# Kernel optimization log

Hardware: AMD Instinct MI355X
Metric: run time of the kernel (lower is better)

## Reference

```python
import jax, jax.numpy as jnp
import numpy as np

NEG = -1000000000.0


def setup_inputs() -> dict:
    key = jax.random.key(0)
    k1, k2, k3, k4, k5 = jax.random.split(key, 5)
    B, T, D, Q = 8, 2048, 1024, 128
    x = jax.random.normal(k1, (B, T, D), dtype=jnp.float32)
    attn_mask = jax.random.randint(k2, (B, T), 0, 2).astype(jnp.bool_)
    s = 1.0 / np.sqrt(D)
    Wq = jax.random.normal(k3, (Q, D), dtype=jnp.float32) * s
    Wk = jax.random.normal(k4, (Q, D), dtype=jnp.float32) * s
    Wv = jax.random.normal(k5, (Q, D), dtype=jnp.float32) * s
    return {"x": x, "attn_mask": attn_mask, "Wq": Wq, "Wk": Wk, "Wv": Wv}


def reference(x, attn_mask, Wq, Wk, Wv):
    # x: (B,T,D); W*: (Q,D) torch Linear weights (y = x @ W.T)
    q = jnp.einsum('btd,qd->btq', x, Wq)
    k = jnp.einsum('btd,qd->btq', x, Wk)
    v = jnp.einsum('btd,qd->btq', x, Wv)
    logits = jnp.einsum('btq,bsq->bts', q, k)  # (B,T,T), no 1/sqrt(d) scaling (matches source)
    m = attn_mask[:, None, :]  # (B,1,T) broadcasts over query dim, == repeat(1,T,1)
    logits = jnp.where(m, logits, NEG)
    A = jax.nn.softmax(logits, axis=-1)
    A = jnp.where(m, A, 0.0)
    return jnp.einsum('bts,bsq->btq', A, v)
```

## Files before the change

### kernel.cpp

```cpp
#include <hip/hip_runtime.h>
#include <hip/hip_bf16.h>
#include <hip/hip_fp16.h>

typedef _Float16 half8 __attribute__((ext_vector_type(8)));
typedef _Float16 half4v __attribute__((ext_vector_type(4)));
typedef float float4v __attribute__((ext_vector_type(4)));

#define MFMA_F16(a, b, c) __builtin_amdgcn_mfma_f32_16x16x32_f16((a), (b), (c), 0, 0, 0)

#define GLDS16(gp, lp) \
    __builtin_amdgcn_global_load_lds((const __attribute__((address_space(1))) unsigned int*)(gp), \
                                     (__attribute__((address_space(3))) unsigned int*)(lp), 16, 0, 0)

#define BATCH 8
#define SEQ   2048
#define DIM   1024
#define QD    128
#define BT    (BATCH * SEQ)
#define NSPLIT 4
#define KSPAN (SEQ / NSPLIT)

__device__ __forceinline__ float dpp_max16(float x) {
    int v;
    v = __builtin_amdgcn_update_dpp(0, __float_as_int(x), 0xB1, 0xF, 0xF, false);
    x = fmaxf(x, __int_as_float(v));
    v = __builtin_amdgcn_update_dpp(0, __float_as_int(x), 0x4E, 0xF, 0xF, false);
    x = fmaxf(x, __int_as_float(v));
    v = __builtin_amdgcn_update_dpp(0, __float_as_int(x), 0x141, 0xF, 0xF, false);
    x = fmaxf(x, __int_as_float(v));
    v = __builtin_amdgcn_update_dpp(0, __float_as_int(x), 0x140, 0xF, 0xF, false);
    x = fmaxf(x, __int_as_float(v));
    return x;
}

__global__ __launch_bounds__(256) void cvt_x_kernel(const float* __restrict__ s,
                                                    _Float16* __restrict__ d) {
    int i = blockIdx.x * 256 + threadIdx.x;
    float4 f = ((const float4*)s)[i];
    half4v h = {(_Float16)f.x, (_Float16)f.y, (_Float16)f.z, (_Float16)f.w};
    ((half4v*)d)[i] = h;
}

__global__ __launch_bounds__(256) void cvt_w_kernel(const float* __restrict__ Wq,
                                                    const float* __restrict__ Wk,
                                                    const float* __restrict__ Wv,
                                                    _Float16* __restrict__ Wh) {
    const float* src = (blockIdx.y == 0) ? Wq : ((blockIdx.y == 1) ? Wk : Wv);
    int i = blockIdx.x * 256 + threadIdx.x;
    float4 f = ((const float4*)src)[i];
    half4v h = {(_Float16)f.x, (_Float16)f.y, (_Float16)f.z, (_Float16)f.w};
    ((half4v*)(Wh + (size_t)blockIdx.y * QD * DIM))[i] = h;
}

__global__ __launch_bounds__(256, 3) void proj_kernel(
    const _Float16* __restrict__ xh,
    const _Float16* __restrict__ Wh,
    _Float16* __restrict__ q_out,
    _Float16* __restrict__ k_out,
    _Float16* __restrict__ vt_out)
{
    __shared__ _Float16 As[64 * 64];
    __shared__ _Float16 Bs[128 * 64];

    const int tid  = threadIdx.x;
    const int lane = tid & 63;
    const int wave = tid >> 6;
    const int quad = lane >> 4;
    const int l15  = lane & 15;
    const int wr   = wave >> 1;
    const int wc   = wave & 1;

    const int which = blockIdx.y;
    const _Float16* W = Wh + (size_t)which * QD * DIM;
    const int row0 = blockIdx.x * 64;

    float4v acc[2][4];
#pragma unroll
    for (int rf = 0; rf < 2; rf++)
#pragma unroll
        for (int n = 0; n < 4; n++)
            acc[rf][n] = (float4v){0.f, 0.f, 0.f, 0.f};

    for (int kk = 0; kk < DIM; kk += 64) {
        __syncthreads();
#pragma unroll
        for (int c = 0; c < 2; c++) {
            int ci = wave * 128 + c * 64 + lane;
            int r  = ci >> 3;
            int g  = (ci & 7) ^ (r & 7);
            GLDS16(xh + (size_t)(row0 + r) * DIM + kk + g * 8, &As[(wave * 128 + c * 64) * 8]);
        }
#pragma unroll
        for (int c = 0; c < 4; c++) {
            int ci = wave * 256 + c * 64 + lane;
            int r  = ci >> 3;
            int g  = (ci & 7) ^ (r & 7);
            GLDS16(W + (size_t)r * DIM + kk + g * 8, &Bs[(wave * 256 + c * 64) * 8]);
        }
        __syncthreads();

        half8 af[2][2], bf[4][2];
#pragma unroll
        for (int rf = 0; rf < 2; rf++)
#pragma unroll
            for (int kc = 0; kc < 2; kc++) {
                int r = wr * 32 + rf * 16 + l15;
                int g = (kc * 4 + quad) ^ (r & 7);
                af[rf][kc] = *(const half8*)&As[r * 64 + g * 8];
            }
#pragma unroll
        for (int n = 0; n < 4; n++)
#pragma unroll
            for (int kc = 0; kc < 2; kc++) {
                int r = wc * 64 + n * 16 + l15;
                int g = (kc * 4 + quad) ^ (r & 7);
                bf[n][kc] = *(const half8*)&Bs[r * 64 + g * 8];
            }
#pragma unroll
        for (int kc = 0; kc < 2; kc++)
#pragma unroll
            for (int rf = 0; rf < 2; rf++)
#pragma unroll
                for (int n = 0; n < 4; n++)
                    acc[rf][n] = MFMA_F16(af[rf][kc], bf[n][kc], acc[rf][n]);
    }

    if (which == 2) {
#pragma unroll
        for (int rf = 0; rf < 2; rf++) {
            int grow0 = row0 + wr * 32 + rf * 16 + quad * 4;
            int b  = grow0 >> 11;
            int t0 = grow0 & 2047;
#pragma unroll
            for (int n = 0; n < 4; n++) {
                int col = wc * 64 + n * 16 + l15;
                half4v h;
#pragma unroll
                for (int r = 0; r < 4; r++) h[r] = (_Float16)acc[rf][n][r];
                *(half4v*)&vt_out[((size_t)(b * QD + col)) * SEQ + t0] = h;
            }
        }
    } else {
        _Float16* out = (which == 0) ? q_out : k_out;
#pragma unroll
        for (int rf = 0; rf < 2; rf++) {
            int grow0 = row0 + wr * 32 + rf * 16 + quad * 4;
#pragma unroll
            for (int n = 0; n < 4; n++) {
                int col = wc * 64 + n * 16 + l15;
#pragma unroll
                for (int r = 0; r < 4; r++)
                    out[(size_t)(grow0 + r) * QD + col] = (_Float16)acc[rf][n][r];
            }
        }
    }
}

__global__ __launch_bounds__(256, 2) void attn_kernel(
    const _Float16* __restrict__ q,
    const _Float16* __restrict__ k,
    const _Float16* __restrict__ vt,
    const int* __restrict__ mask,
    _Float16* __restrict__ Op,
    float2* __restrict__ ml)
{
    __shared__ _Float16 Ks[64 * 128];
    __shared__ _Float16 Vs[128 * 64];
    __shared__ _Float16 Ps[4 * 32 * 64];
    __shared__ int Ms[64];

    const int tid  = threadIdx.x;
    const int lane = tid & 63;
    const int wave = tid >> 6;
    const int quad = lane >> 4;
    const int l15  = lane & 15;

    const int b  = blockIdx.y;
    const int z  = blockIdx.z;
    const int rowbase = blockIdx.x * 128 + wave * 32;

    half8 qf[2][4];
#pragma unroll
    for (int rf = 0; rf < 2; rf++) {
        const _Float16* qrow = q + ((size_t)(b * SEQ + rowbase + rf * 16 + l15)) * QD + quad * 8;
#pragma unroll
        for (int kc = 0; kc < 4; kc++)
            qf[rf][kc] = *(const half8*)(qrow + kc * 32);
    }

    const half8 onesv = {(_Float16)1, (_Float16)1, (_Float16)1, (_Float16)1,
                         (_Float16)1, (_Float16)1, (_Float16)1, (_Float16)1};

    float4v oacc[2][8];
#pragma unroll
    for (int rf = 0; rf < 2; rf++)
#pragma unroll
        for (int n = 0; n < 8; n++)
            oacc[rf][n] = (float4v){0.f, 0.f, 0.f, 0.f};
    float4v lacc[2] = {(float4v){0.f, 0.f, 0.f, 0.f}, (float4v){0.f, 0.f, 0.f, 0.f}};
    float mrow[2][4];
#pragma unroll
    for (int rf = 0; rf < 2; rf++)
#pragma unroll
        for (int r = 0; r < 4; r++) mrow[rf][r] = -1e30f;

    _Float16* Pw = &Ps[wave * 32 * 64];

    for (int sb = z * KSPAN; sb < z * KSPAN + KSPAN; sb += 64) {
        __syncthreads();
#pragma unroll
        for (int c = 0; c < 4; c++) {
            int ci = wave * 256 + c * 64 + lane;
            int r  = ci >> 4;
            int gs = ci & 15;
            int g  = (gs & 8) | ((gs ^ r) & 7);
            GLDS16(k + ((size_t)(b * SEQ + sb + r)) * QD + g * 8, &Ks[(wave * 256 + c * 64) * 8]);
        }
#pragma unroll
        for (int c = 0; c < 4; c++) {
            int ci = wave * 256 + c * 64 + lane;
            int r  = ci >> 3;
            int g  = ((ci & 7) ^ r) & 7;
            GLDS16(vt + ((size_t)(b * QD + r)) * SEQ + sb + g * 8, &Vs[(wave * 256 + c * 64) * 8]);
        }
        if (tid < 64) Ms[tid] = mask[b * SEQ + sb + tid];
        __syncthreads();

        float4v sacc[2][4];
#pragma unroll
        for (int rf = 0; rf < 2; rf++)
#pragma unroll
            for (int j = 0; j < 4; j++)
                sacc[rf][j] = (float4v){0.f, 0.f, 0.f, 0.f};
#pragma unroll
        for (int kc = 0; kc < 4; kc++) {
            half8 kf[4];
#pragma unroll
            for (int j = 0; j < 4; j++) {
                int r  = j * 16 + l15;
                int g  = kc * 4 + quad;
                int gs = (g & 8) | ((g ^ r) & 7);
                kf[j] = *(const half8*)&Ks[r * 128 + gs * 8];
            }
#pragma unroll
            for (int rf = 0; rf < 2; rf++)
#pragma unroll
                for (int j = 0; j < 4; j++)
                    sacc[rf][j] = MFMA_F16(qf[rf][kc], kf[j], sacc[rf][j]);
        }

        float alpha[2][4];
#pragma unroll
        for (int rf = 0; rf < 2; rf++) {
            float rmax[4] = {-1e30f, -1e30f, -1e30f, -1e30f};
#pragma unroll
            for (int j = 0; j < 4; j++) {
                bool m_ok = (Ms[j * 16 + l15] != 0);
#pragma unroll
                for (int r = 0; r < 4; r++) {
                    float s = m_ok ? sacc[rf][j][r] : -1e30f;
                    sacc[rf][j][r] = s;
                    rmax[r] = fmaxf(rmax[r], s);
                }
            }
#pragma unroll
            for (int r = 0; r < 4; r++) {
                float rm = dpp_max16(rmax[r]);
                float mnew = fmaxf(mrow[rf][r], rm);
                alpha[rf][r] = __expf(mrow[rf][r] - mnew);
                mrow[rf][r] = mnew;
            }
        }

#pragma unroll
        for (int rf = 0; rf < 2; rf++)
#pragma unroll
            for (int j = 0; j < 4; j++) {
                int col = j * 16 + l15;
                int gc  = col >> 3;
#pragma unroll
                for (int r = 0; r < 4; r++) {
                    int m  = rf * 16 + quad * 4 + r;
                    int gs = (gc ^ m) & 7;
                    float s = sacc[rf][j][r];
                    float p = (s > -1e29f) ? __expf(s - mrow[rf][r]) : 0.f;
                    Pw[m * 64 + gs * 8 + (col & 7)] = (_Float16)p;
                }
            }

#pragma unroll
        for (int rf = 0; rf < 2; rf++) {
#pragma unroll
            for (int n = 0; n < 8; n++)
#pragma unroll
                for (int r = 0; r < 4; r++)
                    oacc[rf][n][r] *= alpha[rf][r];
#pragma unroll
            for (int r = 0; r < 4; r++) lacc[rf][r] *= alpha[rf][r];
        }

#pragma unroll
        for (int kc = 0; kc < 2; kc++) {
            half8 pf[2];
#pragma unroll
            for (int rf = 0; rf < 2; rf++) {
                int m  = rf * 16 + l15;
                int gs = ((kc * 4 + quad) ^ m) & 7;
                pf[rf] = *(const half8*)&Pw[m * 64 + gs * 8];
            }
#pragma unroll
            for (int n = 0; n < 8; n++) {
                int r  = n * 16 + l15;
                int gs = ((kc * 4 + quad) ^ r) & 7;
                half8 vf = *(const half8*)&Vs[r * 64 + gs * 8];
#pragma unroll
                for (int rf = 0; rf < 2; rf++)
                    oacc[rf][n] = MFMA_F16(pf[rf], vf, oacc[rf][n]);
            }
#pragma unroll
            for (int rf = 0; rf < 2; rf++)
                lacc[rf] = MFMA_F16(pf[rf], onesv, lacc[rf]);
        }
    }

    _Float16* Oz = Op + (size_t)z * BT * QD;
#pragma unroll
    for (int rf = 0; rf < 2; rf++) {
#pragma unroll
        for (int n = 0; n < 8; n++) {
            int col = n * 16 + l15;
#pragma unroll
            for (int r = 0; r < 4; r++) {
                int row = rowbase + rf * 16 + quad * 4 + r;
                Oz[((size_t)(b * SEQ + row)) * QD + col] = (_Float16)oacc[rf][n][r];
            }
        }
        if (l15 == 0) {
#pragma unroll
            for (int r = 0; r < 4; r++) {
                int row = rowbase + rf * 16 + quad * 4 + r;
                ml[(size_t)z * BT + b * SEQ + row] = make_float2(mrow[rf][r], lacc[rf][r]);
            }
        }
    }
}

__global__ __launch_bounds__(256) void merge_kernel(
    const _Float16* __restrict__ Op,
    const float2* __restrict__ ml,
    float* __restrict__ out)
{
    int gid = blockIdx.x * 256 + threadIdx.x;
    int row = gid >> 4;
    int c8  = (gid & 15) * 8;

    float2 a[NSPLIT];
    float m = -3.0e38f;
#pragma unroll
    for (int s = 0; s < NSPLIT; s++) { a[s] = ml[(size_t)s * BT + row]; m = fmaxf(m, a[s].x); }
    float sc[NSPLIT];
    float denom = 0.f;
#pragma unroll
    for (int s = 0; s < NSPLIT; s++) { sc[s] = __expf(a[s].x - m); denom += sc[s] * a[s].y; }
    float inv = (denom > 0.f) ? (1.0f / denom) : 0.f;

    float acc[8] = {0, 0, 0, 0, 0, 0, 0, 0};
#pragma unroll
    for (int s = 0; s < NSPLIT; s++) {
        half8 o = *(const half8*)&Op[(size_t)s * BT * QD + (size_t)row * QD + c8];
#pragma unroll
        for (int e = 0; e < 8; e++) acc[e] += (float)o[e] * sc[s];
    }
    float4 lo = make_float4(acc[0] * inv, acc[1] * inv, acc[2] * inv, acc[3] * inv);
    float4 hi = make_float4(acc[4] * inv, acc[5] * inv, acc[6] * inv, acc[7] * inv);
    *(float4*)&out[(size_t)row * QD + c8] = lo;
    *(float4*)&out[(size_t)row * QD + c8 + 4] = hi;
}

extern "C" void kernel_launch(void* const* d_in, const int* in_sizes, int n_in,
                              void* d_out, int out_size, void* d_ws, size_t ws_size,
                              hipStream_t stream) {
    const float* x    = (const float*)d_in[0];
    const int*   mask = (const int*)d_in[1];
    const float* Wq   = (const float*)d_in[2];
    const float* Wk   = (const float*)d_in[3];
    const float* Wv   = (const float*)d_in[4];
    float* out = (float*)d_out;

    char* p = (char*)d_ws;
    _Float16* xh  = (_Float16*)p; p += (size_t)BT * DIM * 2;
    _Float16* Wh  = (_Float16*)p; p += (size_t)3 * QD * DIM * 2;
    _Float16* qb  = (_Float16*)p; p += (size_t)BT * QD * 2;
    _Float16* kb  = (_Float16*)p; p += (size_t)BT * QD * 2;
    _Float16* vtb = (_Float16*)p; p += (size_t)BT * QD * 2;
    _Float16* Op  = (_Float16*)p; p += (size_t)NSPLIT * BT * QD * 2;
    float2*   ml  = (float2*)p;

    cvt_x_kernel<<<dim3(BT * DIM / 4 / 256), 256, 0, stream>>>(x, xh);
    cvt_w_kernel<<<dim3(QD * DIM / 4 / 256, 3), 256, 0, stream>>>(Wq, Wk, Wv, Wh);
    proj_kernel<<<dim3(BT / 64, 3), 256, 0, stream>>>(xh, Wh, qb, kb, vtb);
    attn_kernel<<<dim3(SEQ / 128, BATCH, NSPLIT), 256, 0, stream>>>(qb, kb, vtb, mask, Op, ml);
    merge_kernel<<<dim3(BT * 16 / 256), 256, 0, stream>>>(Op, ml, out);
}
```

Before: 164.9 us.

## Fuse x fp32-to-fp16 conversion into projection and use additive mask bias

Removes the standalone x conversion kernel and its fp16 workspace buffer. The projection kernel now loads fp32 x rows into registers, converts them, and writes them to swizzled LDS, replacing the async global-to-LDS copies for the A tile. This drops a full read/write pass over x and one launch. The cost is that each of the three projection blocks reads fp32 x itself, and those register loads replace async LDS loads. Separately, the attention mask is stored as an additive 0/-1e30 bias, which removes the selects before the max and the exp.

```diff
diff --git a/kernel.cpp b/kernel.cpp
--- a/kernel.cpp
+++ b/kernel.cpp
@@ -33,14 +33,6 @@
     return x;
 }
 
-__global__ __launch_bounds__(256) void cvt_x_kernel(const float* __restrict__ s,
-                                                    _Float16* __restrict__ d) {
-    int i = blockIdx.x * 256 + threadIdx.x;
-    float4 f = ((const float4*)s)[i];
-    half4v h = {(_Float16)f.x, (_Float16)f.y, (_Float16)f.z, (_Float16)f.w};
-    ((half4v*)d)[i] = h;
-}
-
 __global__ __launch_bounds__(256) void cvt_w_kernel(const float* __restrict__ Wq,
                                                     const float* __restrict__ Wk,
                                                     const float* __restrict__ Wv,
@@ -53,7 +45,7 @@
 }
 
 __global__ __launch_bounds__(256, 3) void proj_kernel(
-    const _Float16* __restrict__ xh,
+    const float* __restrict__ x,
     const _Float16* __restrict__ Wh,
     _Float16* __restrict__ q_out,
     _Float16* __restrict__ k_out,
@@ -74,6 +66,14 @@
     const _Float16* W = Wh + (size_t)which * QD * DIM;
     const int row0 = blockIdx.x * 64;
 
+    const int ar  = tid >> 2;
+    const int ac4 = tid & 3;
+    const float4* xp = (const float4*)(x + (size_t)(row0 + ar) * DIM) + ac4 * 4;
+    const int ga = ac4 * 2;
+    const int sw = ar & 7;
+    _Float16* aw0 = &As[ar * 64 + ((ga     ^ sw) * 8)];
+    _Float16* aw1 = &As[ar * 64 + (((ga|1) ^ sw) * 8)];
+
     float4v acc[2][4];
 #pragma unroll
     for (int rf = 0; rf < 2; rf++)
@@ -82,14 +82,12 @@
             acc[rf][n] = (float4v){0.f, 0.f, 0.f, 0.f};
 
     for (int kk = 0; kk < DIM; kk += 64) {
+        int kb = kk >> 2;
+        float4 a0 = xp[kb + 0];
+        float4 a1 = xp[kb + 1];
+        float4 a2 = xp[kb + 2];
+        float4 a3 = xp[kb + 3];
         __syncthreads();
-#pragma unroll
-        for (int c = 0; c < 2; c++) {
-            int ci = wave * 128 + c * 64 + lane;
-            int r  = ci >> 3;
-            int g  = (ci & 7) ^ (r & 7);
-            GLDS16(xh + (size_t)(row0 + r) * DIM + kk + g * 8, &As[(wave * 128 + c * 64) * 8]);
-        }
 #pragma unroll
         for (int c = 0; c < 4; c++) {
             int ci = wave * 256 + c * 64 + lane;
@@ -97,6 +95,13 @@
             int g  = (ci & 7) ^ (r & 7);
             GLDS16(W + (size_t)r * DIM + kk + g * 8, &Bs[(wave * 256 + c * 64) * 8]);
         }
+        half8 h0, h1;
+        h0[0] = (_Float16)a0.x; h0[1] = (_Float16)a0.y; h0[2] = (_Float16)a0.z; h0[3] = (_Float16)a0.w;
+        h0[4] = (_Float16)a1.x; h0[5] = (_Float16)a1.y; h0[6] = (_Float16)a1.z; h0[7] = (_Float16)a1.w;
+        h1[0] = (_Float16)a2.x; h1[1] = (_Float16)a2.y; h1[2] = (_Float16)a2.z; h1[3] = (_Float16)a2.w;
+        h1[4] = (_Float16)a3.x; h1[5] = (_Float16)a3.y; h1[6] = (_Float16)a3.z; h1[7] = (_Float16)a3.w;
+        *(half8*)aw0 = h0;
+        *(half8*)aw1 = h1;
         __syncthreads();
 
         half8 af[2][2], bf[4][2];
@@ -167,7 +172,7 @@
     __shared__ _Float16 Ks[64 * 128];
     __shared__ _Float16 Vs[128 * 64];
     __shared__ _Float16 Ps[4 * 32 * 64];
-    __shared__ int Ms[64];
+    __shared__ float Msf[64];
 
     const int tid  = threadIdx.x;
     const int lane = tid & 63;
@@ -223,7 +228,7 @@
             int g  = ((ci & 7) ^ r) & 7;
             GLDS16(vt + ((size_t)(b * QD + r)) * SEQ + sb + g * 8, &Vs[(wave * 256 + c * 64) * 8]);
         }
-        if (tid < 64) Ms[tid] = mask[b * SEQ + sb + tid];
+        if (tid < 64) Msf[tid] = mask[b * SEQ + sb + tid] ? 0.f : -1e30f;
         __syncthreads();
 
         float4v sacc[2][4];
@@ -255,10 +260,10 @@
             float rmax[4] = {-1e30f, -1e30f, -1e30f, -1e30f};
 #pragma unroll
             for (int j = 0; j < 4; j++) {
-                bool m_ok = (Ms[j * 16 + l15] != 0);
+                float bias = Msf[j * 16 + l15];
 #pragma unroll
                 for (int r = 0; r < 4; r++) {
-                    float s = m_ok ? sacc[rf][j][r] : -1e30f;
+                    float s = sacc[rf][j][r] + bias;
                     sacc[rf][j][r] = s;
                     rmax[r] = fmaxf(rmax[r], s);
                 }
@@ -282,8 +287,7 @@
                 for (int r = 0; r < 4; r++) {
                     int m  = rf * 16 + quad * 4 + r;
                     int gs = (gc ^ m) & 7;
-                    float s = sacc[rf][j][r];
-                    float p = (s > -1e29f) ? __expf(s - mrow[rf][r]) : 0.f;
+                    float p = __expf(sacc[rf][j][r] - mrow[rf][r]);
                     Pw[m * 64 + gs * 8 + (col & 7)] = (_Float16)p;
                 }
             }
@@ -388,7 +392,6 @@
     float* out = (float*)d_out;
 
     char* p = (char*)d_ws;
-    _Float16* xh  = (_Float16*)p; p += (size_t)BT * DIM * 2;
     _Float16* Wh  = (_Float16*)p; p += (size_t)3 * QD * DIM * 2;
     _Float16* qb  = (_Float16*)p; p += (size_t)BT * QD * 2;
     _Float16* kb  = (_Float16*)p; p += (size_t)BT * QD * 2;
@@ -396,9 +399,8 @@
     _Float16* Op  = (_Float16*)p; p += (size_t)NSPLIT * BT * QD * 2;
     float2*   ml  = (float2*)p;
 
-    cvt_x_kernel<<<dim3(BT * DIM / 4 / 256), 256, 0, stream>>>(x, xh);
     cvt_w_kernel<<<dim3(QD * DIM / 4 / 256, 3), 256, 0, stream>>>(Wq, Wk, Wv, Wh);
-    proj_kernel<<<dim3(BT / 64, 3), 256, 0, stream>>>(xh, Wh, qb, kb, vtb);
+    proj_kernel<<<dim3(BT / 64, 3), 256, 0, stream>>>(x, Wh, qb, kb, vtb);
     attn_kernel<<<dim3(SEQ / 128, BATCH, NSPLIT), 256, 0, stream>>>(qb, kb, vtb, mask, Op, ml);
     merge_kernel<<<dim3(BT * 16 / 256), 256, 0, stream>>>(Op, ml, out);
 }
```

Result: no change. 163.9 us (-0.6%).
